# Optimization experiments

Measured on AMD Instinct MI355X. Metric: run time of the kernel, lower is better.

The kernel has to match this reference:

```python
import jax, jax.numpy as jnp
import numpy as np

D_IN, D_HIDDEN, DT_RANK, D_MEM, STEP = 256, 64, 16, 128, 16
B_, L_ = 2, 2048
S = 0.02  # weight init scale

def generate_a(d_in, d_hidden):
    i = jnp.arange(d_in, dtype=jnp.float32)[:, None]
    j = jnp.arange(d_hidden, dtype=jnp.float32)[None, :]
    off = jnp.sqrt(2.0 * i + 1.0) * jnp.sqrt(2.0 * j + 1.0)
    return jnp.where(i == j, i + 1.0, jnp.where(i > j, off, 0.0))

def setup_inputs():
    key = jax.random.key(0)
    ks = jax.random.split(key, 10)
    d_out = 3 * D_HIDDEN + 2 * D_IN + 2 * DT_RANK
    return {
        "x": jax.random.normal(ks[0], (B_, L_, D_IN), jnp.float32),
        "W_xproj": jax.random.normal(ks[1], (D_IN, d_out), jnp.float32) * S,
        "W_dt": jax.random.normal(ks[2], (DT_RANK, D_IN), jnp.float32) * S,
        "b_dt": jnp.full((D_IN,), -11.0, jnp.float32),
        "W_dtl": jax.random.normal(ks[3], (DT_RANK, D_IN), jnp.float32) * S,
        "b_dtl": jnp.full((D_IN,), -11.0, jnp.float32),
        "A": generate_a(D_IN, D_HIDDEN),
        "Dp": jnp.ones((D_IN,), jnp.float32),
        "W_Q": jax.random.normal(ks[4], (D_IN, D_MEM), jnp.float32) * S,
        "b_Q": jnp.zeros((D_MEM,), jnp.float32),
        "W_K": jax.random.normal(ks[5], (D_IN, D_MEM), jnp.float32) * S,
        "b_K": jnp.zeros((D_MEM,), jnp.float32),
        "W_V": jax.random.normal(ks[6], (D_IN, D_MEM), jnp.float32) * S,
        "b_V": jnp.zeros((D_MEM,), jnp.float32),
        "W_O": jax.random.normal(ks[7], (D_MEM, D_IN), jnp.float32) * S,
        "b_O": jnp.zeros((D_IN,), jnp.float32),
    }

def _selective_scan(u, delta, A, Bm, Cm, Dp):
    # u, delta: (b,l,d); A: (d,n); Bm, Cm: (b,l,n)
    dA = jnp.exp(jnp.einsum('bld,dn->bldn', delta, A))          # (b,l,d,n)
    dBu = delta[..., None] * Bm[:, :, None, :] * u[..., None]   # (b,l,d,n)
    def comb(e1, e2):
        a1, b1 = e1
        a2, b2 = e2
        return a2 * a1, a2 * b1 + b2
    _, xs = jax.lax.associative_scan(comb, (dA, dBu), axis=1)   # states (b,l,d,n)
    y = jnp.einsum('bldn,bln->bld', xs, Cm)
    if Dp is not None:
        y = y + u * Dp
    return y

def reference(x, W_xproj, W_dt, b_dt, W_dtl, b_dtl, A, Dp, W_Q, b_Q, W_K, b_K, W_V, b_V, W_O, b_O):
    proj = x @ W_xproj  # (b,l,3n+2d+2r)
    splits = np.cumsum([D_HIDDEN, D_HIDDEN, D_HIDDEN, D_IN, D_IN, DT_RANK]).tolist()
    Bm, Bl, Cm, E, Fg, dt, dtl = jnp.split(proj, splits, axis=-1)
    delta = jax.nn.softplus(dt @ W_dt + b_dt)       # delta_softplus=True folded in
    delta_l = jax.nn.softplus(dtl @ W_dtl + b_dtl)
    y = _selective_scan(x, delta, A, Bm, Cm, Dp)
    y_local = _selective_scan(x, delta_l, A, Bl, jnp.ones_like(Bl), None)  # C=ones, D=None
    memory = y_local[:, ::STEP, :]                  # strided checkpoints (b,m,d)
    Q = x @ W_Q + b_Q
    K = memory @ W_K + b_K
    V = memory @ W_V + b_V
    # note: original scales by sqrt(d_hidden), not sqrt(d_memory)
    w = jax.nn.softmax(jnp.einsum('blm,bkm->blk', Q, K) / jnp.sqrt(jnp.float32(D_HIDDEN)), axis=-1)
    att = jnp.einsum('blk,bkm->blm', w, V) @ W_O + b_O
    return y + att * E + x * Fg
```

## Files before the change

kernel.cpp:

```cpp
#include <hip/hip_runtime.h>
#include <math.h>

#define D_INN 256
#define D_HID 64
#define DTR 16
#define D_MEMM 128
#define BB 2
#define LL 2048
#define NROWS (BB*LL)
#define NPROJ 736
#define NTOT 864
#define SEG 16
#define SEGLEN (LL/SEG)
#define NCHUNK (LL/8)

typedef __attribute__((ext_vector_type(8))) short short8v;
typedef __attribute__((ext_vector_type(4))) float float4v;
typedef __attribute__((ext_vector_type(2))) float float2v;

static __device__ __forceinline__ unsigned short f2bf(float f) {
    unsigned int u = __float_as_uint(f);
    u += 0x7fff + ((u >> 16) & 1);
    return (unsigned short)(u >> 16);
}

static __device__ __forceinline__ float rdlane(float v, int l) {
    return __uint_as_float(__builtin_amdgcn_readlane(__float_as_uint(v), l));
}

static __device__ __forceinline__ float2v pk_fma(float2v a, float2v b, float2v c) {
    float2v d;
    asm("v_pk_fma_f32 %0, %1, %2, %3" : "=v"(d) : "v"(a), "v"(b), "v"(c));
    return d;
}
static __device__ __forceinline__ float2v pk_mul(float2v a, float2v b) {
    float2v d;
    asm("v_pk_mul_f32 %0, %1, %2" : "=v"(d) : "v"(a), "v"(b));
    return d;
}
static __device__ __forceinline__ float2v pk_add(float2v a, float2v b) {
    float2v d;
    asm("v_pk_add_f32 %0, %1, %2" : "=v"(d) : "v"(a), "v"(b));
    return d;
}

#define PK(g, b, chunk, n, li) (((((size_t)(g)*BB + (b)) * NCHUNK + (chunk)) * 64 + (n)) * 8 + (li))

__global__ __launch_bounds__(256) void k_gemm(const float* __restrict__ x,
        const float* __restrict__ Wx, const float* __restrict__ Wq,
        const float* __restrict__ bq, float* __restrict__ proj,
        float* __restrict__ packed) {
    __shared__ unsigned short As[64][40];
    __shared__ unsigned short Bs[64][40];
    const int t = threadIdx.x;
    const int lane = t & 63, w = t >> 6;
    const int wr = w >> 1, wc = w & 1;
    const int row0 = blockIdx.y * 64, col0 = blockIdx.x * 64;

    float4v acc[2][2];
    #pragma unroll
    for (int i = 0; i < 2; i++)
        #pragma unroll
        for (int j = 0; j < 2; j++) acc[i][j] = (float4v)0.f;

    const int ar = t >> 2, akq = (t & 3) * 8;
    const int bk = t >> 3, bcq = (t & 7) * 8;

    for (int k0 = 0; k0 < D_INN; k0 += 32) {
        float4 a0 = *(const float4*)&x[(size_t)(row0 + ar) * D_INN + k0 + akq];
        float4 a1 = *(const float4*)&x[(size_t)(row0 + ar) * D_INN + k0 + akq + 4];
        float4 b0 = {}, b1 = {};
        int col = col0 + bcq;
        if (col + 8 <= NPROJ) {
            b0 = *(const float4*)&Wx[(size_t)(k0 + bk) * NPROJ + col];
            b1 = *(const float4*)&Wx[(size_t)(k0 + bk) * NPROJ + col + 4];
        } else if (col < NTOT) {
            b0 = *(const float4*)&Wq[(size_t)(k0 + bk) * D_MEMM + (col - NPROJ)];
            b1 = *(const float4*)&Wq[(size_t)(k0 + bk) * D_MEMM + (col - NPROJ) + 4];
        }
        __syncthreads();
        {
            unsigned short av[8] = { f2bf(a0.x), f2bf(a0.y), f2bf(a0.z), f2bf(a0.w),
                                     f2bf(a1.x), f2bf(a1.y), f2bf(a1.z), f2bf(a1.w) };
            *(short8v*)&As[ar][akq] = *(short8v*)av;
            Bs[bcq + 0][bk] = f2bf(b0.x); Bs[bcq + 1][bk] = f2bf(b0.y);
            Bs[bcq + 2][bk] = f2bf(b0.z); Bs[bcq + 3][bk] = f2bf(b0.w);
            Bs[bcq + 4][bk] = f2bf(b1.x); Bs[bcq + 5][bk] = f2bf(b1.y);
            Bs[bcq + 6][bk] = f2bf(b1.z); Bs[bcq + 7][bk] = f2bf(b1.w);
        }
        __syncthreads();
        short8v af[2], bf[2];
        const int fr = lane & 15, fk = (lane >> 4) * 8;
        af[0] = *(short8v*)&As[wr * 32 + fr][fk];
        af[1] = *(short8v*)&As[wr * 32 + 16 + fr][fk];
        bf[0] = *(short8v*)&Bs[wc * 32 + fr][fk];
        bf[1] = *(short8v*)&Bs[wc * 32 + 16 + fr][fk];
        #pragma unroll
        for (int i = 0; i < 2; i++)
            #pragma unroll
            for (int j = 0; j < 2; j++)
                acc[i][j] = __builtin_amdgcn_mfma_f32_16x16x32_bf16(af[i], bf[j], acc[i][j], 0, 0, 0);
    }
    #pragma unroll
    for (int i = 0; i < 2; i++)
        #pragma unroll
        for (int j = 0; j < 2; j++) {
            int cc = col0 + wc * 32 + j * 16 + (lane & 15);
            int rr0 = row0 + wr * 32 + i * 16 + (lane >> 4) * 4;
            if (cc < 192) {
                int g = cc >> 6, n = cc & 63;
                int bb = rr0 >> 11, l = rr0 & (LL - 1);
                float4 pk = make_float4(acc[i][j][0], acc[i][j][1], acc[i][j][2], acc[i][j][3]);
                *(float4*)&packed[PK(g, bb, l >> 3, n, l & 7)] = pk;
            } else {
                #pragma unroll
                for (int e = 0; e < 4; e++) {
                    float v = acc[i][j][e];
                    if (cc >= NPROJ) v += bq[cc - NPROJ];
                    proj[(size_t)(rr0 + e) * NTOT + cc] = v;
                }
            }
        }
}

__global__ __launch_bounds__(256) void k_prep(const float* __restrict__ x,
        const float* __restrict__ proj,
        const float* __restrict__ Wdt, const float* __restrict__ bdt,
        const float* __restrict__ Wdtl, const float* __restrict__ bdtl,
        float* __restrict__ deltaT, float* __restrict__ deltalT,
        float* __restrict__ xT) {
    __shared__ float sh[64 * 66];
    const int t = threadIdx.x;
    if (blockIdx.y == 0) {
        float (*sdt)[17]  = (float(*)[17])sh;
        float (*sdtl)[17] = (float(*)[17])(sh + 16 * 17);
        const int r0 = blockIdx.x * 16;
        const int b = r0 >> 11, l0 = r0 & (LL - 1);
        {
            int r = t >> 4, c = t & 15;
            sdt[r][c]  = proj[(size_t)(r0 + r) * NTOT + 704 + c];
            sdtl[r][c] = proj[(size_t)(r0 + r) * NTOT + 720 + c];
        }
        __syncthreads();
        float w1[DTR], w2[DTR];
        #pragma unroll
        for (int r = 0; r < DTR; r++) {
            w1[r] = Wdt[r * D_INN + t];
            w2[r] = Wdtl[r * D_INN + t];
        }
        const float b1 = bdt[t], b2 = bdtl[t];
        float o1[16], o2[16];
        #pragma unroll
        for (int row = 0; row < 16; ++row) {
            float a1 = b1, a2 = b2;
            #pragma unroll
            for (int r = 0; r < DTR; r++) {
                a1 += sdt[row][r] * w1[r];
                a2 += sdtl[row][r] * w2[r];
            }
            o1[row] = (a1 > 20.f) ? a1 : log1pf(expf(a1));
            o2[row] = (a2 > 20.f) ? a2 : log1pf(expf(a2));
        }
        float* p1 = &deltaT[((size_t)b * D_INN + t) * LL + l0];
        float* p2 = &deltalT[((size_t)b * D_INN + t) * LL + l0];
        #pragma unroll
        for (int j = 0; j < 16; j += 4) {
            *(float4*)&p1[j] = make_float4(o1[j], o1[j+1], o1[j+2], o1[j+3]);
            *(float4*)&p2[j] = make_float4(o2[j], o2[j+1], o2[j+2], o2[j+3]);
        }
    } else {
        float (*tile)[65] = (float(*)[65])sh;
        const int bx = blockIdx.x;
        const int lt = (bx & 31) * 64, dt = ((bx >> 5) & 3) * 64, b = bx >> 7;
        const int c = t & 63, rg = (t >> 6) * 16;
        #pragma unroll
        for (int j = 0; j < 16; ++j)
            tile[rg + j][c] = x[((size_t)b * LL + lt + rg + j) * D_INN + dt + c];
        __syncthreads();
        #pragma unroll
        for (int j = 0; j < 16; ++j)
            xT[((size_t)b * D_INN + dt + rg + j) * LL + lt + c] = tile[c][rg + j];
    }
}

__global__ __launch_bounds__(256) void k_scanA(const float* __restrict__ xT,
        const float* __restrict__ packed, const float* __restrict__ A,
        const float* __restrict__ deltaT, const float* __restrict__ deltalT,
        float* __restrict__ Qbuf, float* __restrict__ SDbuf,
        float* __restrict__ cumd, float* __restrict__ mem) {
    const int t = threadIdx.x, w = t >> 6, n = t & 63;
    const int b = blockIdx.y, seg = blockIdx.z;
    const int d = blockIdx.x * 4 + w;
    const int lr = n & 7;
    const float Aln = A[d * D_HID + n] * 1.44269504f;
    const float2v Aln2 = {Aln, Aln};
    const float* uT  = xT + ((size_t)b * D_INN + d) * LL + seg * SEGLEN;
    const float* dT0 = deltaT + ((size_t)b * D_INN + d) * LL + seg * SEGLEN;
    const float* dT1 = deltalT + ((size_t)b * D_INN + d) * LL + seg * SEGLEN;
    const float* Bp0 = packed + PK(0, b, seg * 16, 0, 0);
    const float* Bp1 = packed + PK(1, b, seg * 16, 0, 0);

    float cum[8], part[8];
    float2v s01 = {0.f, 0.f}, sd01 = {0.f, 0.f};

    for (int c = 0; c < 16; ++c) {
        float u   = uT[c * 8 + lr];
        float dv0 = dT0[c * 8 + lr];
        float dv1 = dT1[c * 8 + lr];
        float pl0 = dv0 * u, pl1 = dv1 * u;
        float4 B00 = *(const float4*)&Bp0[((size_t)c * 64 + n) * 8];
        float4 B01 = *(const float4*)&Bp0[((size_t)c * 64 + n) * 8 + 4];
        float4 B10 = *(const float4*)&Bp1[((size_t)c * 64 + n) * 8];
        float4 B11 = *(const float4*)&Bp1[((size_t)c * 64 + n) * 8 + 4];
        float Bv0[8] = {B00.x, B00.y, B00.z, B00.w, B01.x, B01.y, B01.z, B01.w};
        float Bv1[8] = {B10.x, B10.y, B10.z, B10.w, B11.x, B11.y, B11.z, B11.w};

        float2v dv01[8], dA01[8], pB01[8];
        #pragma unroll
        for (int li = 0; li < 8; ++li) {
            dv01[li] = (float2v){rdlane(dv0, li), rdlane(dv1, li)};
            float2v m = pk_mul(dv01[li], Aln2);
            dA01[li] = (float2v){exp2f(m.x), exp2f(m.y)};
            float2v p = (float2v){rdlane(pl0, li), rdlane(pl1, li)};
            pB01[li] = pk_mul(p, (float2v){Bv0[li], Bv1[li]});
        }
        #pragma unroll
        for (int li = 0; li < 8; ++li) {
            s01 = pk_fma(dA01[li], s01, pB01[li]);
            sd01 = pk_add(sd01, dv01[li]);
            if (li == 0 && (c & 1) == 0) {
                float v = s01.y;
                #pragma unroll
                for (int off = 32; off >= 1; off >>= 1) v += __shfl_xor(v, off);
                part[c >> 1] = v;
                cum[c >> 1] = sd01.y;
            }
        }
    }

    Qbuf[(((size_t)b * SEG + seg) * D_INN + d) * 64 + n] = s01.x;
    Qbuf[(((size_t)(2 + b) * SEG + seg) * D_INN + d) * 64 + n] = s01.y;
    if (n == 0) {
        SDbuf[((size_t)b * SEG + seg) * D_INN + d] = sd01.x;
        SDbuf[((size_t)(2 + b) * SEG + seg) * D_INN + d] = sd01.y;
        #pragma unroll
        for (int ck = 0; ck < 8; ++ck) {
            mem[((size_t)b * 128 + seg * 8 + ck) * D_INN + d] = part[ck];
            cumd[(((size_t)b * SEG + seg) * 8 + ck) * D_INN + d] = cum[ck];
        }
    }
}

__global__ __launch_bounds__(256) void k_scanBC(const float* __restrict__ xT,
        const float* __restrict__ packed, const float* __restrict__ A,
        const float* __restrict__ Dp, const float* __restrict__ deltaT,
        const float* __restrict__ Qbuf, const float* __restrict__ SDbuf,
        const float* __restrict__ cumd,
        float* __restrict__ y, float* __restrict__ mem) {
    __shared__ float rbuf[4][8][65];
    const int t = threadIdx.x, w = t >> 6, n = t & 63;
    const int b = blockIdx.y, seg = blockIdx.z;
    const int d = blockIdx.x * 4 + w;
    const int lr = n & 7, rli = n >> 3, g = n & 7;
    const float Aln = A[d * D_HID + n] * 1.44269504f;
    const float Dpv = Dp[d];
    const size_t rowbase = (size_t)b * LL + (size_t)seg * SEGLEN;
    const float* uT  = xT + ((size_t)b * D_INN + d) * LL + seg * SEGLEN;
    const float* dT0 = deltaT + ((size_t)b * D_INN + d) * LL + seg * SEGLEN;
    const float* Bp = packed + PK(0, b, seg * 16, 0, 0);
    const float* Cp = packed + PK(2, b, seg * 16, 0, 0);

    float sin0 = 0.f, sin1 = 0.f;
    for (int k = 0; k < seg; ++k) {
        float sdk0 = SDbuf[((size_t)b * SEG + k) * D_INN + d];
        float qk0  = Qbuf[(((size_t)b * SEG + k) * D_INN + d) * 64 + n];
        sin0 = fmaf(exp2f(sdk0 * Aln), sin0, qk0);
        float sdk1 = SDbuf[((size_t)(2 + b) * SEG + k) * D_INN + d];
        float qk1  = Qbuf[(((size_t)(2 + b) * SEG + k) * D_INN + d) * 64 + n];
        sin1 = fmaf(exp2f(sdk1 * Aln), sin1, qk1);
    }

    if (seg > 0) {
        #pragma unroll
        for (int ck = 0; ck < 8; ++ck) {
            float cum = cumd[(((size_t)b * SEG + seg) * 8 + ck) * D_INN + d];
            float v = exp2f(cum * Aln) * sin1;
            #pragma unroll
            for (int off = 32; off >= 1; off >>= 1) v += __shfl_xor(v, off);
            if (n == 0) mem[((size_t)b * 128 + seg * 8 + ck) * D_INN + d] += v;
        }
    }

    float s = sin0;
    for (int c = 0; c < 16; ++c) {
        const size_t l0 = rowbase + c * 8;
        float dvl = dT0[c * 8 + lr];
        float uvl = uT[c * 8 + lr];
        float pl = dvl * uvl;
        float4 B0 = *(const float4*)&Bp[((size_t)c * 64 + n) * 8];
        float4 B1 = *(const float4*)&Bp[((size_t)c * 64 + n) * 8 + 4];
        float4 C0 = *(const float4*)&Cp[((size_t)c * 64 + n) * 8];
        float4 C1 = *(const float4*)&Cp[((size_t)c * 64 + n) * 8 + 4];
        float Bv[8] = {B0.x, B0.y, B0.z, B0.w, B1.x, B1.y, B1.z, B1.w};
        float Cv[8] = {C0.x, C0.y, C0.z, C0.w, C1.x, C1.y, C1.z, C1.w};
        float dAr[8], pBr[8];
        #pragma unroll
        for (int li = 0; li < 8; ++li) {
            dAr[li] = exp2f(rdlane(dvl, li) * Aln);
            pBr[li] = rdlane(pl, li) * Bv[li];
        }
        #pragma unroll
        for (int li = 0; li < 8; ++li) {
            s = fmaf(dAr[li], s, pBr[li]);
            rbuf[w][li][n] = s * Cv[li];
        }
        float acc = 0.f;
        #pragma unroll
        for (int j = 0; j < 8; ++j) acc += rbuf[w][rli][g * 8 + j];
        acc += __shfl_xor(acc, 1);
        acc += __shfl_xor(acc, 2);
        acc += __shfl_xor(acc, 4);
        float uv = __shfl(uvl, rli);
        if (g == 0) {
            y[(l0 + rli) * D_INN + d] = acc + uv * Dpv;
        }
    }
}

__global__ __launch_bounds__(128) void k_kvwo(const float* __restrict__ mem,
        const float* __restrict__ Wk, const float* __restrict__ bk,
        const float* __restrict__ Wv, const float* __restrict__ bv,
        const float* __restrict__ Wo,
        float* __restrict__ KT, float* __restrict__ VWo) {
    __shared__ float mrow[256];
    __shared__ float vrow[128];
    const int k = blockIdx.x, b = blockIdx.y;
    const int t = threadIdx.x;
    const float* mr = mem + ((size_t)b * 128 + k) * D_INN;
    mrow[t] = mr[t];
    mrow[t + 128] = mr[t + 128];
    __syncthreads();
    float aK = bk[t], aV = bv[t];
    for (int dd = 0; dd < D_INN; dd++) {
        float m = mrow[dd];
        aK += m * Wk[dd * D_MEMM + t];
        aV += m * Wv[dd * D_MEMM + t];
    }
    KT[((size_t)b * 128 + t) * 128 + k] = aK;
    vrow[t] = aV;
    __syncthreads();
    float a0 = 0.f, a1 = 0.f;
    for (int m = 0; m < 128; ++m) {
        float vm = vrow[m];
        a0 += vm * Wo[(size_t)m * D_INN + t];
        a1 += vm * Wo[(size_t)m * D_INN + t + 128];
    }
    VWo[((size_t)b * 128 + k) * D_INN + t] = a0;
    VWo[((size_t)b * 128 + k) * D_INN + t + 128] = a1;
}

__global__ __launch_bounds__(256) void k_attn(const float* __restrict__ x,
        const float* __restrict__ proj, const float* __restrict__ y,
        const float* __restrict__ KT, const float* __restrict__ VWo,
        const float* __restrict__ bo, float* __restrict__ out) {
    __shared__ float qs[8][132];
    __shared__ float ws[8][132];
    __shared__ float denom[8];
    const int t = threadIdx.x;
    const int b = blockIdx.y;
    const int r0 = blockIdx.x * 8;
    const size_t rowbase = (size_t)b * LL + r0;
    {
        int r = t >> 5, c4 = (t & 31) * 4;
        *(float4*)&qs[r][c4] = *(const float4*)&proj[(rowbase + r) * NTOT + NPROJ + c4];
    }
    __syncthreads();
    {
        const int kk = t & 127, rg = (t >> 7) * 4;
        const float* KTb = KT + (size_t)b * 128 * 128 + kk;
        float acc[4] = {};
        #pragma unroll 8
        for (int m = 0; m < 128; m += 4) {
            float k0 = KTb[(size_t)m * 128];
            float k1 = KTb[(size_t)(m + 1) * 128];
            float k2 = KTb[(size_t)(m + 2) * 128];
            float k3 = KTb[(size_t)(m + 3) * 128];
            #pragma unroll
            for (int r = 0; r < 4; ++r) {
                float4 qv = *(const float4*)&qs[rg + r][m];
                acc[r] += qv.x * k0 + qv.y * k1 + qv.z * k2 + qv.w * k3;
            }
        }
        #pragma unroll
        for (int r = 0; r < 4; ++r) ws[rg + r][kk] = acc[r] * 0.125f;
    }
    __syncthreads();
    {
        const int r = t >> 5, j = t & 31;
        float4 v0 = *(float4*)&ws[r][j * 4];
        float mx = fmaxf(fmaxf(v0.x, v0.y), fmaxf(v0.z, v0.w));
        #pragma unroll
        for (int o = 1; o < 32; o <<= 1) mx = fmaxf(mx, __shfl_xor(mx, o));
        v0.x = expf(v0.x - mx); v0.y = expf(v0.y - mx);
        v0.z = expf(v0.z - mx); v0.w = expf(v0.w - mx);
        float sum = v0.x + v0.y + v0.z + v0.w;
        #pragma unroll
        for (int o = 1; o < 32; o <<= 1) sum += __shfl_xor(sum, o);
        *(float4*)&ws[r][j * 4] = v0;
        if (j == 0) denom[r] = sum;
    }
    __syncthreads();
    {
        const int w = t >> 6, lane = t & 63;
        const int c0 = lane * 4;
        const float* vb = VWo + (size_t)b * 128 * D_INN + c0;
        float acc[2][4] = {};
        #pragma unroll 8
        for (int k = 0; k < 128; k += 2) {
            float4 vw0 = *(const float4*)&vb[(size_t)k * D_INN];
            float4 vw1 = *(const float4*)&vb[(size_t)(k + 1) * D_INN];
            #pragma unroll
            for (int r = 0; r < 2; ++r) {
                float wk0 = ws[w * 2 + r][k];
                float wk1 = ws[w * 2 + r][k + 1];
                acc[r][0] += wk0 * vw0.x + wk1 * vw1.x;
                acc[r][1] += wk0 * vw0.y + wk1 * vw1.y;
                acc[r][2] += wk0 * vw0.z + wk1 * vw1.z;
                acc[r][3] += wk0 * vw0.w + wk1 * vw1.w;
            }
        }
        float4 bov = *(const float4*)&bo[c0];
        #pragma unroll
        for (int r = 0; r < 2; ++r) {
            size_t rr = rowbase + w * 2 + r;
            float dn = 1.f / denom[w * 2 + r];
            float4 yv = *(const float4*)&y[rr * D_INN + c0];
            float4 xv = *(const float4*)&x[rr * D_INN + c0];
            float4 Ev = *(const float4*)&proj[rr * NTOT + 192 + c0];
            float4 Fv = *(const float4*)&proj[rr * NTOT + 448 + c0];
            float4 o;
            o.x = yv.x + (acc[r][0] * dn + bov.x) * Ev.x + xv.x * Fv.x;
            o.y = yv.y + (acc[r][1] * dn + bov.y) * Ev.y + xv.y * Fv.y;
            o.z = yv.z + (acc[r][2] * dn + bov.z) * Ev.z + xv.z * Fv.z;
            o.w = yv.w + (acc[r][3] * dn + bov.w) * Ev.w + xv.w * Fv.w;
            *(float4*)&out[rr * D_INN + c0] = o;
        }
    }
}

extern "C" void kernel_launch(void* const* d_in, const int* in_sizes, int n_in,
                              void* d_out, int out_size, void* d_ws, size_t ws_size,
                              hipStream_t stream) {
    const float* x    = (const float*)d_in[0];
    const float* Wx   = (const float*)d_in[1];
    const float* Wdt  = (const float*)d_in[2];
    const float* bdt  = (const float*)d_in[3];
    const float* Wdtl = (const float*)d_in[4];
    const float* bdtl = (const float*)d_in[5];
    const float* A    = (const float*)d_in[6];
    const float* Dp   = (const float*)d_in[7];
    const float* Wq   = (const float*)d_in[8];
    const float* bq   = (const float*)d_in[9];
    const float* Wk   = (const float*)d_in[10];
    const float* bk   = (const float*)d_in[11];
    const float* Wv   = (const float*)d_in[12];
    const float* bv   = (const float*)d_in[13];
    const float* Wo   = (const float*)d_in[14];
    const float* bo   = (const float*)d_in[15];
    float* out = (float*)d_out;
    float* ws = (float*)d_ws;

    float* proj    = ws;
    float* deltaT  = proj + (size_t)NROWS * NTOT;
    float* deltalT = deltaT + (size_t)NROWS * D_INN;
    float* yb      = deltalT + (size_t)NROWS * D_INN;
    float* mem     = yb + (size_t)NROWS * D_INN;
    float* KTb     = mem + (size_t)BB * 128 * D_INN;
    float* Qbuf    = KTb + (size_t)BB * 128 * D_MEMM;
    float* SDbuf   = Qbuf + (size_t)4 * SEG * D_INN * 64;
    float* cumd    = SDbuf + (size_t)4 * SEG * D_INN;
    float* VWo     = cumd + (size_t)BB * SEG * 8 * D_INN;
    float* xT      = VWo + (size_t)BB * 128 * D_INN;
    float* packed  = xT + (size_t)NROWS * D_INN;

    hipLaunchKernelGGL(k_gemm, dim3(14, 64), dim3(256), 0, stream, x, Wx, Wq, bq, proj, packed);
    hipLaunchKernelGGL(k_prep, dim3(256, 2), dim3(256), 0, stream,
                       x, proj, Wdt, bdt, Wdtl, bdtl, deltaT, deltalT, xT);
    hipLaunchKernelGGL(k_scanA, dim3(64, 2, 16), dim3(256), 0, stream,
                       xT, packed, A, deltaT, deltalT, Qbuf, SDbuf, cumd, mem);
    hipLaunchKernelGGL(k_scanBC, dim3(64, 2, 16), dim3(256), 0, stream,
                       xT, packed, A, Dp, deltaT, Qbuf, SDbuf, cumd, yb, mem);
    hipLaunchKernelGGL(k_kvwo, dim3(128, 2), dim3(128), 0, stream,
                       mem, Wk, bk, Wv, bv, Wo, KTb, VWo);
    hipLaunchKernelGGL(k_attn, dim3(LL / 8, 2), dim3(256), 0, stream,
                       x, proj, yb, KTb, VWo, bo, out);
}
```

Measured before the change: 192.1 us.

## Precompute delta*u and chunk delta sums in prep, drop readlane broadcasts in scans

The prep kernel now also writes transposed delta*x products for both scans and per-8-step chunk sums of delta. The scan kernels read those values with uniform float4 loads instead of a per-lane load followed by readlane broadcasts, and the packed-FMA helpers are replaced with scalar fmaf. The goal is to cut the cross-lane readlane/SALU traffic and the repeated multiplies inside the serial scan loop. In exchange, prep writes two more full-size arrays that the scans must read back, and the packed f32 math is lost.

```diff
diff --git a/kernel.cpp b/kernel.cpp
--- a/kernel.cpp
+++ b/kernel.cpp
@@ -16,32 +16,11 @@
 
 typedef __attribute__((ext_vector_type(8))) short short8v;
 typedef __attribute__((ext_vector_type(4))) float float4v;
-typedef __attribute__((ext_vector_type(2))) float float2v;
 
 static __device__ __forceinline__ unsigned short f2bf(float f) {
     unsigned int u = __float_as_uint(f);
     u += 0x7fff + ((u >> 16) & 1);
     return (unsigned short)(u >> 16);
-}
-
-static __device__ __forceinline__ float rdlane(float v, int l) {
-    return __uint_as_float(__builtin_amdgcn_readlane(__float_as_uint(v), l));
-}
-
-static __device__ __forceinline__ float2v pk_fma(float2v a, float2v b, float2v c) {
-    float2v d;
-    asm("v_pk_fma_f32 %0, %1, %2, %3" : "=v"(d) : "v"(a), "v"(b), "v"(c));
-    return d;
-}
-static __device__ __forceinline__ float2v pk_mul(float2v a, float2v b) {
-    float2v d;
-    asm("v_pk_mul_f32 %0, %1, %2" : "=v"(d) : "v"(a), "v"(b));
-    return d;
-}
-static __device__ __forceinline__ float2v pk_add(float2v a, float2v b) {
-    float2v d;
-    asm("v_pk_add_f32 %0, %1, %2" : "=v"(d) : "v"(a), "v"(b));
-    return d;
 }
 
 #define PK(g, b, chunk, n, li) (((((size_t)(g)*BB + (b)) * NCHUNK + (chunk)) * 64 + (n)) * 8 + (li))
@@ -128,6 +107,8 @@
         const float* __restrict__ Wdt, const float* __restrict__ bdt,
         const float* __restrict__ Wdtl, const float* __restrict__ bdtl,
         float* __restrict__ deltaT, float* __restrict__ deltalT,
+        float* __restrict__ pT0, float* __restrict__ pT1,
+        float* __restrict__ csum0, float* __restrict__ csum1,
         float* __restrict__ xT) {
     __shared__ float sh[64 * 66];
     const int t = threadIdx.x;
@@ -149,7 +130,7 @@
             w2[r] = Wdtl[r * D_INN + t];
         }
         const float b1 = bdt[t], b2 = bdtl[t];
-        float o1[16], o2[16];
+        float o1[16], o2[16], q1[16], q2[16];
         #pragma unroll
         for (int row = 0; row < 16; ++row) {
             float a1 = b1, a2 = b2;
@@ -160,14 +141,28 @@
             }
             o1[row] = (a1 > 20.f) ? a1 : log1pf(expf(a1));
             o2[row] = (a2 > 20.f) ? a2 : log1pf(expf(a2));
-        }
-        float* p1 = &deltaT[((size_t)b * D_INN + t) * LL + l0];
-        float* p2 = &deltalT[((size_t)b * D_INN + t) * LL + l0];
+            float xv = x[(size_t)(r0 + row) * D_INN + t];
+            q1[row] = o1[row] * xv;
+            q2[row] = o2[row] * xv;
+        }
+        float* d1 = &deltaT[((size_t)b * D_INN + t) * LL + l0];
+        float* d2 = &deltalT[((size_t)b * D_INN + t) * LL + l0];
+        float* p1 = &pT0[((size_t)b * D_INN + t) * LL + l0];
+        float* p2 = &pT1[((size_t)b * D_INN + t) * LL + l0];
         #pragma unroll
         for (int j = 0; j < 16; j += 4) {
-            *(float4*)&p1[j] = make_float4(o1[j], o1[j+1], o1[j+2], o1[j+3]);
-            *(float4*)&p2[j] = make_float4(o2[j], o2[j+1], o2[j+2], o2[j+3]);
-        }
+            *(float4*)&d1[j] = make_float4(o1[j], o1[j+1], o1[j+2], o1[j+3]);
+            *(float4*)&d2[j] = make_float4(o2[j], o2[j+1], o2[j+2], o2[j+3]);
+            *(float4*)&p1[j] = make_float4(q1[j], q1[j+1], q1[j+2], q1[j+3]);
+            *(float4*)&p2[j] = make_float4(q2[j], q2[j+1], q2[j+2], q2[j+3]);
+        }
+        float c0a = 0.f, c0b = 0.f, c1a = 0.f, c1b = 0.f;
+        #pragma unroll
+        for (int j = 0; j < 8; ++j) { c0a += o1[j]; c0b += o1[8 + j];
+                                      c1a += o2[j]; c1b += o2[8 + j]; }
+        size_t cbase = ((size_t)b * D_INN + t) * NCHUNK + (l0 >> 3);
+        csum0[cbase] = c0a; csum0[cbase + 1] = c0b;
+        csum1[cbase] = c1a; csum1[cbase + 1] = c1b;
     } else {
         float (*tile)[65] = (float(*)[65])sh;
         const int bx = blockIdx.x;
@@ -183,66 +178,73 @@
     }
 }
 
-__global__ __launch_bounds__(256) void k_scanA(const float* __restrict__ xT,
+__global__ __launch_bounds__(256) void k_scanA(
         const float* __restrict__ packed, const float* __restrict__ A,
         const float* __restrict__ deltaT, const float* __restrict__ deltalT,
+        const float* __restrict__ pT0, const float* __restrict__ pT1,
+        const float* __restrict__ csum0, const float* __restrict__ csum1,
         float* __restrict__ Qbuf, float* __restrict__ SDbuf,
         float* __restrict__ cumd, float* __restrict__ mem) {
     const int t = threadIdx.x, w = t >> 6, n = t & 63;
     const int b = blockIdx.y, seg = blockIdx.z;
     const int d = blockIdx.x * 4 + w;
-    const int lr = n & 7;
     const float Aln = A[d * D_HID + n] * 1.44269504f;
-    const float2v Aln2 = {Aln, Aln};
-    const float* uT  = xT + ((size_t)b * D_INN + d) * LL + seg * SEGLEN;
-    const float* dT0 = deltaT + ((size_t)b * D_INN + d) * LL + seg * SEGLEN;
-    const float* dT1 = deltalT + ((size_t)b * D_INN + d) * LL + seg * SEGLEN;
+    const size_t base = ((size_t)b * D_INN + d) * LL + seg * SEGLEN;
+    const float* dT0 = deltaT + base;
+    const float* dT1 = deltalT + base;
+    const float* pp0 = pT0 + base;
+    const float* pp1 = pT1 + base;
     const float* Bp0 = packed + PK(0, b, seg * 16, 0, 0);
     const float* Bp1 = packed + PK(1, b, seg * 16, 0, 0);
+    const size_t cbase = ((size_t)b * D_INN + d) * NCHUNK + seg * 16;
 
     float cum[8], part[8];
-    float2v s01 = {0.f, 0.f}, sd01 = {0.f, 0.f};
+    float s0 = 0.f, s1 = 0.f, sd1 = 0.f;
 
     for (int c = 0; c < 16; ++c) {
-        float u   = uT[c * 8 + lr];
-        float dv0 = dT0[c * 8 + lr];
-        float dv1 = dT1[c * 8 + lr];
-        float pl0 = dv0 * u, pl1 = dv1 * u;
+        float4 d0a = *(const float4*)&dT0[c * 8], d0b = *(const float4*)&dT0[c * 8 + 4];
+        float4 d1a = *(const float4*)&dT1[c * 8], d1b = *(const float4*)&dT1[c * 8 + 4];
+        float4 p0a = *(const float4*)&pp0[c * 8], p0b = *(const float4*)&pp0[c * 8 + 4];
+        float4 p1a = *(const float4*)&pp1[c * 8], p1b = *(const float4*)&pp1[c * 8 + 4];
         float4 B00 = *(const float4*)&Bp0[((size_t)c * 64 + n) * 8];
         float4 B01 = *(const float4*)&Bp0[((size_t)c * 64 + n) * 8 + 4];
         float4 B10 = *(const float4*)&Bp1[((size_t)c * 64 + n) * 8];
         float4 B11 = *(const float4*)&Bp1[((size_t)c * 64 + n) * 8 + 4];
+        float dv0[8] = {d0a.x, d0a.y, d0a.z, d0a.w, d0b.x, d0b.y, d0b.z, d0b.w};
+        float dv1[8] = {d1a.x, d1a.y, d1a.z, d1a.w, d1b.x, d1b.y, d1b.z, d1b.w};
+        float pv0[8] = {p0a.x, p0a.y, p0a.z, p0a.w, p0b.x, p0b.y, p0b.z, p0b.w};
+        float pv1[8] = {p1a.x, p1a.y, p1a.z, p1a.w, p1b.x, p1b.y, p1b.z, p1b.w};
         float Bv0[8] = {B00.x, B00.y, B00.z, B00.w, B01.x, B01.y, B01.z, B01.w};
         float Bv1[8] = {B10.x, B10.y, B10.z, B10.w, B11.x, B11.y, B11.z, B11.w};
-
-        float2v dv01[8], dA01[8], pB01[8];
         #pragma unroll
         for (int li = 0; li < 8; ++li) {
-            dv01[li] = (float2v){rdlane(dv0, li), rdlane(dv1, li)};
-            float2v m = pk_mul(dv01[li], Aln2);
-            dA01[li] = (float2v){exp2f(m.x), exp2f(m.y)};
-            float2v p = (float2v){rdlane(pl0, li), rdlane(pl1, li)};
-            pB01[li] = pk_mul(p, (float2v){Bv0[li], Bv1[li]});
-        }
-        #pragma unroll
-        for (int li = 0; li < 8; ++li) {
-            s01 = pk_fma(dA01[li], s01, pB01[li]);
-            sd01 = pk_add(sd01, dv01[li]);
+            s0 = fmaf(exp2f(dv0[li] * Aln), s0, pv0[li] * Bv0[li]);
+            s1 = fmaf(exp2f(dv1[li] * Aln), s1, pv1[li] * Bv1[li]);
             if (li == 0 && (c & 1) == 0) {
-                float v = s01.y;
+                float v = s1;
                 #pragma unroll
                 for (int off = 32; off >= 1; off >>= 1) v += __shfl_xor(v, off);
                 part[c >> 1] = v;
-                cum[c >> 1] = sd01.y;
+                cum[c >> 1] = sd1 + dv1[0];
             }
         }
-    }
-
-    Qbuf[(((size_t)b * SEG + seg) * D_INN + d) * 64 + n] = s01.x;
-    Qbuf[(((size_t)(2 + b) * SEG + seg) * D_INN + d) * 64 + n] = s01.y;
+        sd1 += csum1[cbase + c];
+    }
+    float sd0 = 0.f;
+    {
+        float4 ca = *(const float4*)&csum0[cbase];
+        float4 cb = *(const float4*)&csum0[cbase + 4];
+        float4 cc = *(const float4*)&csum0[cbase + 8];
+        float4 cd = *(const float4*)&csum0[cbase + 12];
+        sd0 = ((ca.x + ca.y) + (ca.z + ca.w)) + ((cb.x + cb.y) + (cb.z + cb.w))
+            + ((cc.x + cc.y) + (cc.z + cc.w)) + ((cd.x + cd.y) + (cd.z + cd.w));
+    }
+
+    Qbuf[(((size_t)b * SEG + seg) * D_INN + d) * 64 + n] = s0;
+    Qbuf[(((size_t)(2 + b) * SEG + seg) * D_INN + d) * 64 + n] = s1;
     if (n == 0) {
-        SDbuf[((size_t)b * SEG + seg) * D_INN + d] = sd01.x;
-        SDbuf[((size_t)(2 + b) * SEG + seg) * D_INN + d] = sd01.y;
+        SDbuf[((size_t)b * SEG + seg) * D_INN + d] = sd0;
+        SDbuf[((size_t)(2 + b) * SEG + seg) * D_INN + d] = sd1;
         #pragma unroll
         for (int ck = 0; ck < 8; ++ck) {
             mem[((size_t)b * 128 + seg * 8 + ck) * D_INN + d] = part[ck];
@@ -254,6 +256,7 @@
 __global__ __launch_bounds__(256) void k_scanBC(const float* __restrict__ xT,
         const float* __restrict__ packed, const float* __restrict__ A,
         const float* __restrict__ Dp, const float* __restrict__ deltaT,
+        const float* __restrict__ pT0,
         const float* __restrict__ Qbuf, const float* __restrict__ SDbuf,
         const float* __restrict__ cumd,
         float* __restrict__ y, float* __restrict__ mem) {
@@ -265,8 +268,10 @@
     const float Aln = A[d * D_HID + n] * 1.44269504f;
     const float Dpv = Dp[d];
     const size_t rowbase = (size_t)b * LL + (size_t)seg * SEGLEN;
-    const float* uT  = xT + ((size_t)b * D_INN + d) * LL + seg * SEGLEN;
-    const float* dT0 = deltaT + ((size_t)b * D_INN + d) * LL + seg * SEGLEN;
+    const size_t base = ((size_t)b * D_INN + d) * LL + seg * SEGLEN;
+    const float* uT  = xT + base;
+    const float* dT0 = deltaT + base;
+    const float* pp0 = pT0 + base;
     const float* Bp = packed + PK(0, b, seg * 16, 0, 0);
     const float* Cp = packed + PK(2, b, seg * 16, 0, 0);
 
@@ -294,20 +299,22 @@
     float s = sin0;
     for (int c = 0; c < 16; ++c) {
         const size_t l0 = rowbase + c * 8;
-        float dvl = dT0[c * 8 + lr];
+        float4 d0a = *(const float4*)&dT0[c * 8], d0b = *(const float4*)&dT0[c * 8 + 4];
+        float4 p0a = *(const float4*)&pp0[c * 8], p0b = *(const float4*)&pp0[c * 8 + 4];
         float uvl = uT[c * 8 + lr];
-        float pl = dvl * uvl;
         float4 B0 = *(const float4*)&Bp[((size_t)c * 64 + n) * 8];
         float4 B1 = *(const float4*)&Bp[((size_t)c * 64 + n) * 8 + 4];
         float4 C0 = *(const float4*)&Cp[((size_t)c * 64 + n) * 8];
         float4 C1 = *(const float4*)&Cp[((size_t)c * 64 + n) * 8 + 4];
+        float dv[8] = {d0a.x, d0a.y, d0a.z, d0a.w, d0b.x, d0b.y, d0b.z, d0b.w};
+        float pv[8] = {p0a.x, p0a.y, p0a.z, p0a.w, p0b.x, p0b.y, p0b.z, p0b.w};
         float Bv[8] = {B0.x, B0.y, B0.z, B0.w, B1.x, B1.y, B1.z, B1.w};
         float Cv[8] = {C0.x, C0.y, C0.z, C0.w, C1.x, C1.y, C1.z, C1.w};
         float dAr[8], pBr[8];
         #pragma unroll
         for (int li = 0; li < 8; ++li) {
-            dAr[li] = exp2f(rdlane(dvl, li) * Aln);
-            pBr[li] = rdlane(pl, li) * Bv[li];
+            dAr[li] = exp2f(dv[li] * Aln);
+            pBr[li] = pv[li] * Bv[li];
         }
         #pragma unroll
         for (int li = 0; li < 8; ++li) {
@@ -473,7 +480,11 @@
     float* proj    = ws;
     float* deltaT  = proj + (size_t)NROWS * NTOT;
     float* deltalT = deltaT + (size_t)NROWS * D_INN;
-    float* yb      = deltalT + (size_t)NROWS * D_INN;
+    float* pT0     = deltalT + (size_t)NROWS * D_INN;
+    float* pT1     = pT0 + (size_t)NROWS * D_INN;
+    float* csum0   = pT1 + (size_t)NROWS * D_INN;
+    float* csum1   = csum0 + (size_t)BB * D_INN * NCHUNK;
+    float* yb      = csum1 + (size_t)BB * D_INN * NCHUNK;
     float* mem     = yb + (size_t)NROWS * D_INN;
     float* KTb     = mem + (size_t)BB * 128 * D_INN;
     float* Qbuf    = KTb + (size_t)BB * 128 * D_MEMM;
@@ -485,11 +496,13 @@
 
     hipLaunchKernelGGL(k_gemm, dim3(14, 64), dim3(256), 0, stream, x, Wx, Wq, bq, proj, packed);
     hipLaunchKernelGGL(k_prep, dim3(256, 2), dim3(256), 0, stream,
-                       x, proj, Wdt, bdt, Wdtl, bdtl, deltaT, deltalT, xT);
+                       x, proj, Wdt, bdt, Wdtl, bdtl, deltaT, deltalT,
+                       pT0, pT1, csum0, csum1, xT);
     hipLaunchKernelGGL(k_scanA, dim3(64, 2, 16), dim3(256), 0, stream,
-                       xT, packed, A, deltaT, deltalT, Qbuf, SDbuf, cumd, mem);
+                       packed, A, deltaT, deltalT, pT0, pT1, csum0, csum1,
+                       Qbuf, SDbuf, cumd, mem);
     hipLaunchKernelGGL(k_scanBC, dim3(64, 2, 16), dim3(256), 0, stream,
-                       xT, packed, A, Dp, deltaT, Qbuf, SDbuf, cumd, yb, mem);
+                       xT, packed, A, Dp, deltaT, pT0, Qbuf, SDbuf, cumd, yb, mem);
     hipLaunchKernelGGL(k_kvwo, dim3(128, 2), dim3(128), 0, stream,
                        mem, Wk, bk, Wv, bv, Wo, KTb, VWo);
     hipLaunchKernelGGL(k_attn, dim3(LL / 8, 2), dim3(256), 0, stream,
```

Result: slower. 197.5 us, median of 2 (+2.8%).
